# Kernel optimization log

Hardware: AMD Instinct MI355X
Metric: run time of the kernel (lower is better)

The kernel has to match this reference:

```python
import jax, jax.numpy as jnp
import numpy as np

N = 100000   # num_nodes
E = 1000000  # num_edges
H = 64       # hidden_dim
M = 64       # msg_dim
C = 16       # num_classes


def setup_inputs() -> dict:
    key = jax.random.key(0)
    ks = jax.random.split(key, 16)
    s = 1.0 / np.sqrt(H)
    inp = {
        "features": jax.random.normal(ks[0], (N, H), jnp.float32),
        "src": jax.random.randint(ks[1], (E,), 0, N, dtype=jnp.int32),
        "dst": jax.random.randint(ks[2], (E,), 0, N, dtype=jnp.int32),
        "edge_types": jax.random.randint(ks[3], (E,), 0, 2, dtype=jnp.int32) == 1,
        # per-edge-type message linears (edge_matrix[0] for type==True, [1] for type==False)
        "W0": jax.random.uniform(ks[4], (M, H), jnp.float32, -s, s),
        "b0": jax.random.uniform(ks[5], (M,), jnp.float32, -s, s),
        "W1": jax.random.uniform(ks[6], (M, H), jnp.float32, -s, s),
        "b1": jax.random.uniform(ks[7], (M,), jnp.float32, -s, s),
        # GRU (single layer, single step): gates order [r, z, n] as in torch
        "W_ih": jax.random.uniform(ks[8], (3 * H, M), jnp.float32, -s, s),
        "W_hh": jax.random.uniform(ks[9], (3 * H, H), jnp.float32, -s, s),
        "b_ih": jax.random.uniform(ks[10], (3 * H,), jnp.float32, -s, s),
        "b_hh": jax.random.uniform(ks[11], (3 * H,), jnp.float32, -s, s),
        # output classifier
        "W_out": jax.random.uniform(ks[12], (C, H), jnp.float32, -s, s),
        "b_out": jax.random.uniform(ks[13], (C,), jnp.float32, -s, s),
    }
    return inp


def reference(features, src, dst, edge_types,
              W0, b0, W1, b1, W_ih, W_hh, b_ih, b_hh, W_out, b_out):
    # gather source-node features per edge: [E, H]
    x = features[src]
    # tiny per-edge-type linear; select by edge type
    m0 = x @ W0.T + b0            # type True  -> edge_matrix[0]
    m1 = x @ W1.T + b1            # type False -> edge_matrix[1]
    msg = jnp.where(edge_types[:, None], m0, m1)  # [E, M]
    # scatter-add messages into node buffer (zero-initialized accumulator)
    agg = jax.ops.segment_sum(msg, dst, num_segments=N)  # [N, M]
    # single GRU step: input=agg, hidden=features
    gi = agg @ W_ih.T + b_ih       # [N, 3H]
    gh = features @ W_hh.T + b_hh  # [N, 3H]
    i_r, i_z, i_n = jnp.split(gi, 3, axis=-1)
    h_r, h_z, h_n = jnp.split(gh, 3, axis=-1)
    r = jax.nn.sigmoid(i_r + h_r)
    z = jax.nn.sigmoid(i_z + h_z)
    n = jnp.tanh(i_n + r * h_n)
    h = (1.0 - z) * n + z * features  # [N, H]
    # output classifier
    return h @ W_out.T + b_out        # [N, C]
```

## Files before the change

kernel.cpp:

```cpp
#include <hip/hip_runtime.h>


typedef __bf16 bf16x8 __attribute__((ext_vector_type(8)));
typedef float  f32x4  __attribute__((ext_vector_type(4)));
typedef int    i32x4  __attribute__((ext_vector_type(4)));

#define MFMA16 __builtin_amdgcn_mfma_f32_16x16x32_bf16
#define NN   100000
#define EE   1000000
#define BB   782
#define NPB  128
#define ECAP 1600
#define DCAP 48
#define CSTRD 49
#define NB   245
#define NWL  24576

__device__ __forceinline__ float sigmoidf_(float x) {
    return 1.0f / (1.0f + __expf(-x));
}

__device__ __forceinline__ bf16x8 ldw(const __bf16* w, int e) {
    int bo = e * 2;
    bo ^= ((bo >> 7) & 7) << 4;
    return *(const bf16x8*)((const char*)w + bo);
}

__global__ __launch_bounds__(256) void k_init(const unsigned char* __restrict__ et,
                                              const float* __restrict__ feat,
                                              const int* __restrict__ dst,
                                              const float* __restrict__ w0,
                                              const float* __restrict__ w1,
                                              const float* __restrict__ wih,
                                              const float* __restrict__ whh,
                                              const float* __restrict__ wout,
                                              __bf16* __restrict__ featb,
                                              __bf16* __restrict__ wb,
                                              int* __restrict__ hist,
                                              int* __restrict__ flag) {
    int b = blockIdx.x, tid = threadIdx.x;
    if (b == 0) {
        __shared__ int sdet[4];
        const i32x4* p = (const i32x4*)et + tid * 16;
        unsigned acc = 0;
#pragma unroll
        for (int j = 0; j < 16; j++) {
            i32x4 w = p[j];
            acc |= (unsigned)(w[0] | w[1] | w[2] | w[3]) & 0xffffff00u;
        }
        unsigned long long m = __ballot(acc != 0);
        if ((tid & 63) == 0) sdet[tid >> 6] = (m != 0ULL);
        __syncthreads();
        if (tid == 0) *flag = sdet[0] | sdet[1] | sdet[2] | sdet[3];
        return;
    }
    if (b < 133) {
        int i = (b - 1) * 256 + tid;
        float v;
        if      (i < 4096)  v = w0[i];
        else if (i < 8192)  v = w1[i - 4096];
        else if (i < 20480) v = wih[i - 8192];
        else if (i < 32768) v = whh[i - 20480];
        else                v = wout[i - 32768];
        wb[i] = (__bf16)v;
        return;
    }
    if (b >= 6383) {
        __shared__ int cnt[BB];
        int hb = b - 6383;
        for (int i = tid; i < BB; i += 256) cnt[i] = 0;
        __syncthreads();
        long e0 = (long)hb * 4096 + tid * 16;
#pragma unroll
        for (int g = 0; g < 2; g++) {
            long e = e0 + g * 8;
            if (e < EE) {
                i32x4 d0 = *(const i32x4*)(dst + e);
                i32x4 d1 = *(const i32x4*)(dst + e + 4);
#pragma unroll
                for (int j = 0; j < 4; j++) atomicAdd(&cnt[d0[j] >> 7], 1);
#pragma unroll
                for (int j = 0; j < 4; j++) atomicAdd(&cnt[d1[j] >> 7], 1);
            }
        }
        __syncthreads();
        for (int i = tid; i < BB; i += 256) hist[hb * BB + i] = cnt[i];
        return;
    }
    long i = ((long)(b - 133) * 256 + tid) * 4;
    if (i >= (long)NN * 64) return;
    f32x4 v = *(const f32x4*)(feat + i);
    union { __bf16 e[4]; unsigned long long u; } o;
#pragma unroll
    for (int j = 0; j < 4; j++) o.e[j] = (__bf16)v[j];
    *(unsigned long long*)(featb + i) = o.u;
}

__global__ __launch_bounds__(256) void k_s2(const int* __restrict__ hist,
                                            int* __restrict__ blockBase,
                                            int* __restrict__ bucketCnt) {
    int b = blockIdx.x * 4 + (threadIdx.x >> 6);
    int lane = threadIdx.x & 63;
    if (b >= BB) return;
    int carry = 0;
    for (int c = 0; c < 4; c++) {
        int blk = c * 64 + lane;
        int v = (blk < NB) ? hist[blk * BB + b] : 0;
        int x = v;
#pragma unroll
        for (int off = 1; off < 64; off <<= 1) {
            int y = __shfl_up(x, off, 64);
            if (lane >= off) x += y;
        }
        if (blk < NB) blockBase[blk * BB + b] = x - v + carry;
        carry += __shfl(x, 63, 64);
    }
    if (lane == 0) bucketCnt[b] = carry;
}

__global__ __launch_bounds__(512) void k_s3(const int* __restrict__ src,
                                            const int* __restrict__ dst,
                                            const unsigned char* __restrict__ etype,
                                            const int* __restrict__ flag,
                                            const int* __restrict__ blockBase,
                                            int* __restrict__ region) {
    __shared__ int cur[BB];
    int blk = blockIdx.x, tid = threadIdx.x;
    for (int i = tid; i < BB; i += 512) cur[i] = blockBase[blk * BB + i];
    __syncthreads();
    long e0 = (long)blk * 4096 + tid * 8;
    if (e0 >= EE) return;
    i32x4 s0 = *(const i32x4*)(src + e0);
    i32x4 s1 = *(const i32x4*)(src + e0 + 4);
    i32x4 d0 = *(const i32x4*)(dst + e0);
    i32x4 d1 = *(const i32x4*)(dst + e0 + 4);
    int t[8];
    if (*flag) {
        unsigned long long w = *(const unsigned long long*)(etype + e0);
#pragma unroll
        for (int j = 0; j < 8; j++) t[j] = (int)((w >> (8 * j)) & 0xff);
    } else {
        i32x4 w0 = *(const i32x4*)((const int*)etype + e0);
        i32x4 w1 = *(const i32x4*)((const int*)etype + e0 + 4);
#pragma unroll
        for (int j = 0; j < 4; j++) { t[j] = w0[j]; t[4 + j] = w1[j]; }
    }
    int dd[8] = {d0[0], d0[1], d0[2], d0[3], d1[0], d1[1], d1[2], d1[3]};
    int ss[8] = {s0[0], s0[1], s0[2], s0[3], s1[0], s1[1], s1[2], s1[3]};
#pragma unroll
    for (int j = 0; j < 8; j++) {
        int b  = dd[j] >> 7;
        int nl = dd[j] & 127;
        int r  = atomicAdd(&cur[b], 1);
        if (r < ECAP)
            region[b * ECAP + r] = (nl << 18) | ((t[j] ? 1 : 0) << 17) | ss[j];
    }
}

__global__ __launch_bounds__(512)
__attribute__((amdgpu_waves_per_eu(4, 4)))
void k_gm(const __bf16* __restrict__ featb,
          const int* __restrict__ region,
          const int* __restrict__ bucketCnt,
          const float* __restrict__ feat,
          const __bf16* __restrict__ wb,
          const float* __restrict__ b0,
          const float* __restrict__ b1,
          const float* __restrict__ bih,
          const float* __restrict__ bhh,
          const float* __restrict__ bout,
          float* __restrict__ out) {
    __shared__ __align__(16) __bf16 wlds[NWL];
    __shared__ __align__(16) int csr[NPB * CSTRD];
    __shared__ int ncnt[NPB];
    int b = blockIdx.x, tid = threadIdx.x, lane = tid & 63, wave = tid >> 6;
    int L = lane & 15, q = lane >> 4;
    int n0 = b * NPB + wave * 16;

    int cntE = min(bucketCnt[b], ECAP);
    if (tid < NPB) ncnt[tid] = 0;
    __syncthreads();
    const int* reg = region + b * ECAP;
    for (int i = tid; i < cntE; i += 512) {
        int rec = reg[i];
        int nl = rec >> 18;
        int r = atomicAdd(&ncnt[nl], 1);
        if (r < DCAP) csr[nl * CSTRD + r] = rec & 0x3ffff;
    }
    const __bf16* wsrc = wb + 8192;
    for (int k = tid * 8; k < NWL; k += 512 * 8) {
        bf16x8 v = *(const bf16x8*)(wsrc + k);
        int bo = k * 2;
        int so = bo ^ (((bo >> 7) & 7) << 4);
        *(bf16x8*)((char*)wlds + so) = v;
    }
    __syncthreads();

    int nl = wave * 16 + L;
    int cnt = (n0 < NN) ? min(ncnt[nl], DCAP) : 0;
    const int* eb = &csr[nl * CSTRD];

    float sA[16], s1[16];
#pragma unroll
    for (int j = 0; j < 16; j++) { sA[j] = 0.f; s1[j] = 0.f; }
    int c1 = 0;
    int i = 0;
    for (; i + 4 <= cnt; i += 4) {
        int e0v = eb[i], e1v = eb[i + 1], e2v = eb[i + 2], e3v = eb[i + 3];
        const __bf16* r0 = featb + (long)(e0v & 0x1ffff) * 64;
        const __bf16* r1 = featb + (long)(e1v & 0x1ffff) * 64;
        const __bf16* r2 = featb + (long)(e2v & 0x1ffff) * 64;
        const __bf16* r3 = featb + (long)(e3v & 0x1ffff) * 64;
        bf16x8 a0 = *(const bf16x8*)(r0 + q * 8);
        bf16x8 a1 = *(const bf16x8*)(r0 + 32 + q * 8);
        bf16x8 b0v = *(const bf16x8*)(r1 + q * 8);
        bf16x8 b1v = *(const bf16x8*)(r1 + 32 + q * 8);
        bf16x8 c0v = *(const bf16x8*)(r2 + q * 8);
        bf16x8 c1v = *(const bf16x8*)(r2 + 32 + q * 8);
        bf16x8 d0v = *(const bf16x8*)(r3 + q * 8);
        bf16x8 d1v = *(const bf16x8*)(r3 + 32 + q * 8);
        int t0 = (e0v >> 17) & 1, t1 = (e1v >> 17) & 1;
        int t2 = (e2v >> 17) & 1, t3 = (e3v >> 17) & 1;
        c1 += t0 + t1 + t2 + t3;
        float f0 = (float)t0, f1 = (float)t1, f2 = (float)t2, f3 = (float)t3;
#pragma unroll
        for (int j = 0; j < 8; j++) {
            float va = (float)a0[j], wa = (float)a1[j];
            float vb = (float)b0v[j], wb2 = (float)b1v[j];
            sA[j]     += va + vb;
            sA[8 + j] += wa + wb2;
            s1[j]     += f0 * va + f1 * vb;
            s1[8 + j] += f0 * wa + f1 * wb2;
            float vc = (float)c0v[j], wc = (float)c1v[j];
            float vd = (float)d0v[j], wd = (float)d1v[j];
            sA[j]     += vc + vd;
            sA[8 + j] += wc + wd;
            s1[j]     += f2 * vc + f3 * vd;
            s1[8 + j] += f2 * wc + f3 * wd;
        }
    }
    if (i + 2 <= cnt) {
        int ea = eb[i], ebn = eb[i + 1];
        const __bf16* rowa = featb + (long)(ea & 0x1ffff) * 64;
        const __bf16* rowb = featb + (long)(ebn & 0x1ffff) * 64;
        bf16x8 a0 = *(const bf16x8*)(rowa + q * 8);
        bf16x8 a1 = *(const bf16x8*)(rowa + 32 + q * 8);
        bf16x8 b0v = *(const bf16x8*)(rowb + q * 8);
        bf16x8 b1v = *(const bf16x8*)(rowb + 32 + q * 8);
        int ta = (ea >> 17) & 1, tb = (ebn >> 17) & 1;
        c1 += ta + tb;
        float fa = (float)ta, fb = (float)tb;
#pragma unroll
        for (int j = 0; j < 8; j++) {
            float va = (float)a0[j], wa = (float)a1[j];
            float vb = (float)b0v[j], wb2 = (float)b1v[j];
            sA[j]     += va + vb;
            sA[8 + j] += wa + wb2;
            s1[j]     += fa * va + fb * vb;
            s1[8 + j] += fa * wa + fb * wb2;
        }
        i += 2;
    }
    if (i < cnt) {
        int ea = eb[i];
        const __bf16* rowa = featb + (long)(ea & 0x1ffff) * 64;
        bf16x8 a0 = *(const bf16x8*)(rowa + q * 8);
        bf16x8 a1 = *(const bf16x8*)(rowa + 32 + q * 8);
        int ta = (ea >> 17) & 1;
        c1 += ta;
        float fa = (float)ta;
#pragma unroll
        for (int j = 0; j < 8; j++) {
            float va = (float)a0[j], wa = (float)a1[j];
            sA[j] += va;          sA[8 + j] += wa;
            s1[j] += fa * va;     s1[8 + j] += fa * wa;
        }
    }
    if (n0 >= NN) return;

    const __bf16* fr = featb + (long)(n0 + L) * 64;
    bf16x8 Aft[2] = { *(const bf16x8*)(fr + q * 8),
                      *(const bf16x8*)(fr + 32 + q * 8) };

    bf16x8 AS1[2], AS0[2];
    {
        union { bf16x8 v; __bf16 e[8]; } u;
#pragma unroll
        for (int ch = 0; ch < 2; ch++) {
#pragma unroll
            for (int j = 0; j < 8; j++) u.e[j] = (__bf16)s1[ch * 8 + j];
            AS1[ch] = u.v;
#pragma unroll
            for (int j = 0; j < 8; j++) u.e[j] = (__bf16)(sA[ch * 8 + j] - s1[ch * 8 + j]);
            AS0[ch] = u.v;
        }
    }
    int ccp = cnt | (c1 << 16);
    float fc1[4], fc0[4];
#pragma unroll
    for (int r = 0; r < 4; r++) {
        int v = __shfl(ccp, q * 4 + r, 64);
        int c1v = v >> 16;
        fc1[r] = (float)c1v; fc0[r] = (float)((v & 0xffff) - c1v);
    }

    __bf16* sH = (__bf16*)((char*)csr + wave * (16 * CSTRD * 4));
    const __bf16* w0b = wb, * w1b = wb + 4096, * woutb = wb + 32768;
    f32x4 zz = {0.f, 0.f, 0.f, 0.f};

#pragma unroll
    for (int nb = 0; nb < 4; nb++) {
        f32x4 acc = zz;
#pragma unroll
        for (int ch = 0; ch < 2; ch++) {
            int off = (nb * 16 + L) * 64 + ch * 32 + q * 8;
            acc = MFMA16(AS1[ch], *(const bf16x8*)(w0b + off), acc, 0, 0, 0);
            acc = MFMA16(AS0[ch], *(const bf16x8*)(w1b + off), acc, 0, 0, 0);
        }
        float bs0 = b0[nb * 16 + L], bs1 = b1[nb * 16 + L];
#pragma unroll
        for (int r = 0; r < 4; r++)
            sH[(q * 4 + r) * 80 + nb * 16 + L] =
                (__bf16)(acc[r] + fc1[r] * bs0 + fc0[r] * bs1);
    }

    bf16x8 Aag[2];
#pragma unroll
    for (int ch = 0; ch < 2; ch++)
        Aag[ch] = *(const bf16x8*)&sH[L * 80 + ch * 32 + q * 8];

#pragma unroll
    for (int nb = 0; nb < 4; nb++) {
        int row = nb * 16 + L;
        float fvb[4];
#pragma unroll
        for (int r = 0; r < 4; r++)
            fvb[r] = feat[(long)(n0 + q * 4 + r) * 64 + nb * 16 + L];
        f32x4 aR = zz, aZ = zz, aIN = zz, aHN = zz;
#pragma unroll
        for (int ch = 0; ch < 2; ch++) {
            int ko = ch * 32 + q * 8;
            aR  = MFMA16(Aag[ch], ldw(wlds, row * 64 + ko), aR, 0, 0, 0);
            aR  = MFMA16(Aft[ch], ldw(wlds, 12288 + row * 64 + ko), aR, 0, 0, 0);
            aZ  = MFMA16(Aag[ch], ldw(wlds, (64 + row) * 64 + ko), aZ, 0, 0, 0);
            aZ  = MFMA16(Aft[ch], ldw(wlds, 12288 + (64 + row) * 64 + ko), aZ, 0, 0, 0);
            aIN = MFMA16(Aag[ch], ldw(wlds, (128 + row) * 64 + ko), aIN, 0, 0, 0);
            aHN = MFMA16(Aft[ch], ldw(wlds, 12288 + (128 + row) * 64 + ko), aHN, 0, 0, 0);
        }
        int h = row;
        float br  = bih[h] + bhh[h];
        float bz  = bih[64 + h] + bhh[64 + h];
        float bin = bih[128 + h];
        float bhn = bhh[128 + h];
#pragma unroll
        for (int r = 0; r < 4; r++) {
            float rv = sigmoidf_(aR[r] + br);
            float zv = sigmoidf_(aZ[r] + bz);
            float nv = tanhf(aIN[r] + bin + rv * (aHN[r] + bhn));
            float fv = fvb[r];
            sH[(q * 4 + r) * 80 + h] = (__bf16)((1.0f - zv) * nv + zv * fv);
        }
    }

    bf16x8 Ah0 = *(const bf16x8*)&sH[L * 80 + q * 8];
    bf16x8 Ah1 = *(const bf16x8*)&sH[L * 80 + 32 + q * 8];
    bf16x8 Bo0 = *(const bf16x8*)(woutb + L * 64 + q * 8);
    bf16x8 Bo1 = *(const bf16x8*)(woutb + L * 64 + 32 + q * 8);
    f32x4 o = zz;
    o = MFMA16(Ah0, Bo0, o, 0, 0, 0);
    o = MFMA16(Ah1, Bo1, o, 0, 0, 0);
    float bo = bout[L];
#pragma unroll
    for (int r = 0; r < 4; r++)
        out[(long)(n0 + q * 4 + r) * 16 + L] = o[r] + bo;
}

extern "C" void kernel_launch(void* const* d_in, const int* in_sizes, int n_in,
                              void* d_out, int out_size, void* d_ws, size_t ws_size,
                              hipStream_t stream) {
    const float* features = (const float*)d_in[0];
    const int*   src      = (const int*)d_in[1];
    const int*   dst      = (const int*)d_in[2];
    const unsigned char* etype = (const unsigned char*)d_in[3];
    const float* W0   = (const float*)d_in[4];
    const float* b0   = (const float*)d_in[5];
    const float* W1   = (const float*)d_in[6];
    const float* b1   = (const float*)d_in[7];
    const float* Wih  = (const float*)d_in[8];
    const float* Whh  = (const float*)d_in[9];
    const float* bih  = (const float*)d_in[10];
    const float* bhh  = (const float*)d_in[11];
    const float* Wout = (const float*)d_in[12];
    const float* bout = (const float*)d_in[13];
    float* out = (float*)d_out;

    char* ws = (char*)d_ws;
    size_t off = 0;
    __bf16* featb     = (__bf16*)(ws + off); off += (size_t)NN * 64 * 2;
    int*    region    = (int*)(ws + off);    off += (size_t)BB * ECAP * 4;
    int*    hist      = (int*)(ws + off);    off += (size_t)NB * BB * 4;
    int*    blockBase = (int*)(ws + off);    off += (size_t)NB * BB * 4;
    int*    bucketCnt = (int*)(ws + off);    off += (size_t)BB * 4;
    __bf16* wb        = (__bf16*)(ws + off); off += 33792 * 2;
    int*    flag      = (int*)(ws + off);

    k_init<<<6628, 256, 0, stream>>>(etype, features, dst, W0, W1, Wih, Whh,
                                     Wout, featb, wb, hist, flag);
    k_s2<<<(BB + 3) / 4, 256, 0, stream>>>(hist, blockBase, bucketCnt);
    k_s3<<<NB, 512, 0, stream>>>(src, dst, etype, flag, blockBase, region);
    k_gm<<<BB, 512, 0, stream>>>(featb, region, bucketCnt, features, wb,
                                 b0, b1, bih, bhh, bout, out);
}
```

Baseline: 171.4 us.

## Split fused gather+GRU kernel into separate gather and matmul kernels

Splits the fused kernel into two. The first gathers and accumulates per-node feature sums split by edge type, then writes them to global memory as bf16 together with the edge counts. The second loads those sums, stages the weights in LDS and runs the MFMA message, GRU and output stages. The aim is to free the gather phase from the LDS and register pressure of the weight tile so more waves can hide gather latency, at the cost of an extra kernel launch and a global round-trip of about 25MB of intermediates.

```diff
diff --git a/kernel.cpp b/kernel.cpp
--- a/kernel.cpp
+++ b/kernel.cpp
@@ -157,20 +157,12 @@
     }
 }
 
-__global__ __launch_bounds__(512)
-__attribute__((amdgpu_waves_per_eu(4, 4)))
-void k_gm(const __bf16* __restrict__ featb,
-          const int* __restrict__ region,
-          const int* __restrict__ bucketCnt,
-          const float* __restrict__ feat,
-          const __bf16* __restrict__ wb,
-          const float* __restrict__ b0,
-          const float* __restrict__ b1,
-          const float* __restrict__ bih,
-          const float* __restrict__ bhh,
-          const float* __restrict__ bout,
-          float* __restrict__ out) {
-    __shared__ __align__(16) __bf16 wlds[NWL];
+__global__ __launch_bounds__(512) void k_g2(const __bf16* __restrict__ featb,
+                                            const int* __restrict__ region,
+                                            const int* __restrict__ bucketCnt,
+                                            __bf16* __restrict__ s1b,
+                                            __bf16* __restrict__ s0b,
+                                            int* __restrict__ cc) {
     __shared__ __align__(16) int csr[NPB * CSTRD];
     __shared__ int ncnt[NPB];
     int b = blockIdx.x, tid = threadIdx.x, lane = tid & 63, wave = tid >> 6;
@@ -186,13 +178,6 @@
         int nl = rec >> 18;
         int r = atomicAdd(&ncnt[nl], 1);
         if (r < DCAP) csr[nl * CSTRD + r] = rec & 0x3ffff;
-    }
-    const __bf16* wsrc = wb + 8192;
-    for (int k = tid * 8; k < NWL; k += 512 * 8) {
-        bf16x8 v = *(const bf16x8*)(wsrc + k);
-        int bo = k * 2;
-        int so = bo ^ (((bo >> 7) & 7) << 4);
-        *(bf16x8*)((char*)wlds + so) = v;
     }
     __syncthreads();
 
@@ -278,33 +263,66 @@
     }
     if (n0 >= NN) return;
 
-    const __bf16* fr = featb + (long)(n0 + L) * 64;
-    bf16x8 Aft[2] = { *(const bf16x8*)(fr + q * 8),
-                      *(const bf16x8*)(fr + 32 + q * 8) };
-
-    bf16x8 AS1[2], AS0[2];
-    {
-        union { bf16x8 v; __bf16 e[8]; } u;
-#pragma unroll
-        for (int ch = 0; ch < 2; ch++) {
-#pragma unroll
-            for (int j = 0; j < 8; j++) u.e[j] = (__bf16)s1[ch * 8 + j];
-            AS1[ch] = u.v;
-#pragma unroll
-            for (int j = 0; j < 8; j++) u.e[j] = (__bf16)(sA[ch * 8 + j] - s1[ch * 8 + j]);
-            AS0[ch] = u.v;
-        }
-    }
-    int ccp = cnt | (c1 << 16);
+    int n = n0 + L;
+    union { bf16x8 v; __bf16 e[8]; } u;
+#pragma unroll
+    for (int ch = 0; ch < 2; ch++) {
+#pragma unroll
+        for (int j = 0; j < 8; j++) u.e[j] = (__bf16)s1[ch * 8 + j];
+        *(bf16x8*)(s1b + (long)n * 64 + ch * 32 + q * 8) = u.v;
+#pragma unroll
+        for (int j = 0; j < 8; j++) u.e[j] = (__bf16)(sA[ch * 8 + j] - s1[ch * 8 + j]);
+        *(bf16x8*)(s0b + (long)n * 64 + ch * 32 + q * 8) = u.v;
+    }
+    if (q == 0) cc[n] = cnt | (c1 << 16);
+}
+
+__global__ __launch_bounds__(512, 4) void k_m2(const __bf16* __restrict__ s1b,
+                                               const __bf16* __restrict__ s0b,
+                                               const __bf16* __restrict__ featb,
+                                               const float* __restrict__ feat,
+                                               const int* __restrict__ cc,
+                                               const __bf16* __restrict__ wb,
+                                               const float* __restrict__ b0,
+                                               const float* __restrict__ b1,
+                                               const float* __restrict__ bih,
+                                               const float* __restrict__ bhh,
+                                               const float* __restrict__ bout,
+                                               float* __restrict__ out) {
+    __shared__ __align__(16) __bf16 wlds[NWL];
+    __shared__ __align__(16) __bf16 sHall[8][16 * 80];
+    int tid = threadIdx.x, lane = tid & 63, wave = tid >> 6;
+    int L = lane & 15, q = lane >> 4;
+    int n0 = blockIdx.x * NPB + wave * 16;
+
+    bf16x8 AS1[2], AS0[2], Aft[2];
     float fc1[4], fc0[4];
-#pragma unroll
-    for (int r = 0; r < 4; r++) {
-        int v = __shfl(ccp, q * 4 + r, 64);
-        int c1v = v >> 16;
-        fc1[r] = (float)c1v; fc0[r] = (float)((v & 0xffff) - c1v);
-    }
-
-    __bf16* sH = (__bf16*)((char*)csr + wave * (16 * CSTRD * 4));
+    if (n0 < NN) {
+        const __bf16* r1 = s1b + (long)(n0 + L) * 64;
+        const __bf16* r0 = s0b + (long)(n0 + L) * 64;
+        const __bf16* fr = featb + (long)(n0 + L) * 64;
+        AS1[0] = *(const bf16x8*)(r1 + q * 8);  AS1[1] = *(const bf16x8*)(r1 + 32 + q * 8);
+        AS0[0] = *(const bf16x8*)(r0 + q * 8);  AS0[1] = *(const bf16x8*)(r0 + 32 + q * 8);
+        Aft[0] = *(const bf16x8*)(fr + q * 8);  Aft[1] = *(const bf16x8*)(fr + 32 + q * 8);
+        i32x4 cv = *(const i32x4*)(cc + n0 + q * 4);
+#pragma unroll
+        for (int r = 0; r < 4; r++) {
+            int c1 = cv[r] >> 16, ct = cv[r] & 0xffff;
+            fc1[r] = (float)c1; fc0[r] = (float)(ct - c1);
+        }
+    }
+
+    const __bf16* wsrc = wb + 8192;
+    for (int k = tid * 8; k < NWL; k += 512 * 8) {
+        bf16x8 v = *(const bf16x8*)(wsrc + k);
+        int bo = k * 2;
+        int so = bo ^ (((bo >> 7) & 7) << 4);
+        *(bf16x8*)((char*)wlds + so) = v;
+    }
+    __syncthreads();
+    if (n0 >= NN) return;
+
+    __bf16* sH = sHall[wave];
     const __bf16* w0b = wb, * w1b = wb + 4096, * woutb = wb + 32768;
     f32x4 zz = {0.f, 0.f, 0.f, 0.f};
 
@@ -401,6 +419,9 @@
     int*    hist      = (int*)(ws + off);    off += (size_t)NB * BB * 4;
     int*    blockBase = (int*)(ws + off);    off += (size_t)NB * BB * 4;
     int*    bucketCnt = (int*)(ws + off);    off += (size_t)BB * 4;
+    int*    cc        = (int*)(ws + off);    off += (size_t)NN * 4;
+    __bf16* s1b       = (__bf16*)(ws + off); off += (size_t)NN * 64 * 2;
+    __bf16* s0b       = (__bf16*)(ws + off); off += (size_t)NN * 64 * 2;
     __bf16* wb        = (__bf16*)(ws + off); off += 33792 * 2;
     int*    flag      = (int*)(ws + off);
 
@@ -408,6 +429,7 @@
                                      Wout, featb, wb, hist, flag);
     k_s2<<<(BB + 3) / 4, 256, 0, stream>>>(hist, blockBase, bucketCnt);
     k_s3<<<NB, 512, 0, stream>>>(src, dst, etype, flag, blockBase, region);
-    k_gm<<<BB, 512, 0, stream>>>(featb, region, bucketCnt, features, wb,
+    k_g2<<<BB, 512, 0, stream>>>(featb, region, bucketCnt, s1b, s0b, cc);
+    k_m2<<<BB, 512, 0, stream>>>(s1b, s0b, featb, features, cc, wb,
                                  b0, b1, bih, bhh, bout, out);
 }
```

Measured after the change: 185.7 us. 8.3% more time.
